# Optimization experiments

Hardware: AMD Instinct MI355X
Metric: run time of the kernel (lower is better)

Reference implementation:

```python
import jax, jax.numpy as jnp
import numpy as np

N_STEPS = 128
N_UNITS = 2048
BATCH = 256
DT = 1e-3
TAU_M = 10.0 * DT            # NeuroTorch LIFLayer default tau_m
ALPHA = float(np.exp(-DT / TAU_M))  # membrane decay factor
THRESHOLD = 1.0
GAMMA = 100.0                # surrogate-gradient sharpness


@jax.custom_vjp
def heaviside_spike(v):
    # forward: hard threshold; backward: sigmoid surrogate (see fwdbwd module)
    return (v > THRESHOLD).astype(v.dtype)

def _hs_fwd(v):
    return heaviside_spike(v), v

def _hs_bwd(v, g):
    sig = jax.nn.sigmoid(GAMMA * (v - THRESHOLD))
    return (g * GAMMA * sig * (1.0 - sig),)

heaviside_spike.defvjp(_hs_fwd, _hs_bwd)


def setup_inputs() -> dict:
    key = jax.random.key(0)
    kx, kw = jax.random.split(key)
    x = jax.random.normal(kx, (BATCH, N_UNITS), dtype=jnp.float32)
    # LIF feedforward weights (n_units -> n_units), no recurrent connection
    W = (jax.random.normal(kw, (N_UNITS, N_UNITS), dtype=jnp.float32)
         / np.float32(np.sqrt(N_UNITS)))
    return {"x": x, "W": W}


def reference(x, W):
    # x: (B, N) analog input; first "spike" frame is the raw input (as in source).
    def step(carry, _):
        x_fwd, V, Z = carry
        I = x_fwd @ W                                   # (B, N)
        # reset term uses detached spikes in the original (stop_gradient)
        V_next = ALPHA * V * (1.0 - jax.lax.stop_gradient(Z)) + I
        Z_next = heaviside_spike(V_next)
        return (Z_next, V_next, Z_next), Z_next

    V0 = jnp.zeros_like(x)
    Z0 = jnp.zeros_like(x)
    _, spikes = jax.lax.scan(step, (x, V0, Z0), None, length=N_STEPS - 1)
    # spikes: (n_steps-1, B, N); prepend the analog frame -> stack along time
    out = jnp.concatenate([x[None], spikes], axis=0)    # (T, B, N)
    return jnp.transpose(out, (1, 0, 2))                # (B, T, N)
```

## Files before the change

### kernel.cpp

```cpp
#include <hip/hip_runtime.h>
#include <stdint.h>


#define BATCHSZ 256
#define NU      2048
#define TSTEPS  128
#define BLK     1024
#define NWAVES  (BLK / 64)

#define D_BN 128
#define D_BM 8

__global__ __launch_bounds__(128) void lif_dense_v1(
    const float* __restrict__ x,
    const float* __restrict__ W,
    float* __restrict__ ws)
{
    __shared__ float s_x[D_BM * NU];

    const int tid  = threadIdx.x;
    const int lane = tid & 63;
    const int n0   = blockIdx.x * D_BN;
    const int m0   = blockIdx.y * D_BM;

    {
        const float4* xg = (const float4*)(x + (size_t)m0 * NU);
        float4*       xs = (float4*)s_x;
        #pragma unroll
        for (int j = 0; j < 32; ++j)
            xs[j * 128 + tid] = xg[j * 128 + tid];
    }
    __syncthreads();

    const int rb = (tid >> 6) * 4;
    const float* xw = &s_x[rb * NU];

    const float* wp = W + n0 + lane * 2;

    float2 bA[16], bB[16];
    float2 acc[4];
    #pragma unroll
    for (int r = 0; r < 4; ++r) { acc[r].x = 0.0f; acc[r].y = 0.0f; }

    #pragma unroll
    for (int j = 0; j < 16; ++j)
        bA[j] = *(const float2*)(wp + (size_t)j * NU);

    for (int k0 = 0; k0 < NU; k0 += 32) {
        #pragma unroll
        for (int j = 0; j < 16; ++j)
            bB[j] = *(const float2*)(wp + (size_t)(k0 + 16 + j) * NU);

        #pragma unroll
        for (int q = 0; q < 4; ++q) {
            float4 xq[4];
            #pragma unroll
            for (int r = 0; r < 4; ++r)
                xq[r] = *(const float4*)&xw[r * NU + k0 + q * 4];
            const float* xf = (const float*)&xq[0];
            #pragma unroll
            for (int kk = 0; kk < 4; ++kk) {
                float2 wv = bA[q * 4 + kk];
                #pragma unroll
                for (int r = 0; r < 4; ++r) {
                    float xv = xf[r * 4 + kk];
                    acc[r].x = __builtin_fmaf(xv, wv.x, acc[r].x);
                    acc[r].y = __builtin_fmaf(xv, wv.y, acc[r].y);
                }
            }
        }

        if (k0 + 32 < NU) {
            #pragma unroll
            for (int j = 0; j < 16; ++j)
                bA[j] = *(const float2*)(wp + (size_t)(k0 + 32 + j) * NU);
        }

        #pragma unroll
        for (int q = 0; q < 4; ++q) {
            float4 xq[4];
            #pragma unroll
            for (int r = 0; r < 4; ++r)
                xq[r] = *(const float4*)&xw[r * NU + k0 + 16 + q * 4];
            const float* xf = (const float*)&xq[0];
            #pragma unroll
            for (int kk = 0; kk < 4; ++kk) {
                float2 wv = bB[q * 4 + kk];
                #pragma unroll
                for (int r = 0; r < 4; ++r) {
                    float xv = xf[r * 4 + kk];
                    acc[r].x = __builtin_fmaf(xv, wv.x, acc[r].x);
                    acc[r].y = __builtin_fmaf(xv, wv.y, acc[r].y);
                }
            }
        }
    }

    #pragma unroll
    for (int r = 0; r < 4; ++r)
        *(float2*)&ws[(size_t)(m0 + rb + r) * NU + n0 + lane * 2] = acc[r];
}

__global__ __launch_bounds__(BLK) void lif_recurrence(
    const float* __restrict__ x,
    const float* __restrict__ W,
    const float* __restrict__ V1,
    float* __restrict__ out)
{
    const int b    = blockIdx.x;
    const int tid  = threadIdx.x;
    const int lane = tid & 63;
    const int wid  = tid >> 6;

    __shared__ int           s_idx[NU];
    __shared__ unsigned char s_flag[NU];
    __shared__ int           s_wsum[NWAVES];
    __shared__ int           s_cnt;

    const int n0 = tid;
    const int n1 = tid + BLK;

    float* outb = out + (size_t)b * TSTEPS * NU;

    float V0, V1r;
    int   z0, z1;
    {
        float x0 = x[(size_t)b * NU + n0];
        float x1 = x[(size_t)b * NU + n1];
        outb[n0] = x0;
        outb[n1] = x1;
        V0  = V1[(size_t)b * NU + n0];
        V1r = V1[(size_t)b * NU + n1];
        z0 = V0  > 1.0f;
        z1 = V1r > 1.0f;
        float* f1 = outb + NU;
        f1[n0] = z0 ? 1.0f : 0.0f;
        f1[n1] = z1 ? 1.0f : 0.0f;
        s_flag[n0] = (unsigned char)z0;
        s_flag[n1] = (unsigned char)z1;
    }
    __syncthreads();

    for (int t = 2; t < TSTEPS; ++t) {
        int f0 = s_flag[2 * tid];
        int f1 = s_flag[2 * tid + 1];
        int c  = f0 + f1;
        int v  = c;
        #pragma unroll
        for (int d = 1; d < 64; d <<= 1) {
            int o = __shfl_up(v, d);
            if (lane >= d) v += o;
        }
        if (lane == 63) s_wsum[wid] = v;
        __syncthreads();
        int base = 0;
        #pragma unroll
        for (int w = 0; w < NWAVES; ++w) base += (w < wid) ? s_wsum[w] : 0;
        int off = base + v - c;
        if (f0) s_idx[off++] = (2 * tid) * NU;
        if (f1) s_idx[off]   = (2 * tid + 1) * NU;
        if (tid == BLK - 1) s_cnt = base + v;
        __syncthreads();

        int cnt = s_cnt;
        if (cnt == 0) {
            size_t  elems  = (size_t)(TSTEPS - t) * NU;
            float4* p      = (float4*)(outb + (size_t)t * NU);
            int     chunks = (int)(elems / 4);
            float4  zz; zz.x = zz.y = zz.z = zz.w = 0.0f;
            for (int i = tid; i < chunks; i += BLK) p[i] = zz;
            return;
        }

        float I0 = 0.0f, I1 = 0.0f;
        const float* Wc = W + tid;
        int i = 0;
        for (; i + 4 <= cnt; i += 4) {
            const float* r0 = Wc + s_idx[i];
            const float* r1 = Wc + s_idx[i + 1];
            const float* r2 = Wc + s_idx[i + 2];
            const float* r3 = Wc + s_idx[i + 3];
            float a0 = r0[0], b0 = r0[BLK];
            float a1 = r1[0], b1 = r1[BLK];
            float a2 = r2[0], b2 = r2[BLK];
            float a3 = r3[0], b3 = r3[BLK];
            I0 += a0; I0 += a1; I0 += a2; I0 += a3;
            I1 += b0; I1 += b1; I1 += b2; I1 += b3;
        }
        for (; i < cnt; ++i) {
            const float* r = Wc + s_idx[i];
            I0 += r[0];
            I1 += r[BLK];
        }

        float d0 = 0.90483741803595952f * V0;
        float d1 = 0.90483741803595952f * V1r;
        asm volatile("" : "+v"(d0), "+v"(d1));
        float nv0 = (z0 ? 0.0f : d0) + I0;
        float nv1 = (z1 ? 0.0f : d1) + I1;
        V0 = nv0; V1r = nv1;
        z0 = nv0 > 1.0f;
        z1 = nv1 > 1.0f;

        float* po = outb + (size_t)t * NU;
        po[n0] = z0 ? 1.0f : 0.0f;
        po[n1] = z1 ? 1.0f : 0.0f;
        s_flag[n0] = (unsigned char)z0;
        s_flag[n1] = (unsigned char)z1;
        __syncthreads();
    }
}

__global__ __launch_bounds__(BLK) void lif_fused(
    const float* __restrict__ x,
    const float* __restrict__ W,
    float* __restrict__ out)
{
    const int b    = blockIdx.x;
    const int tid  = threadIdx.x;
    const int lane = tid & 63;
    const int wid  = tid >> 6;

    __shared__ float         s_x[NU];
    __shared__ int           s_idx[NU];
    __shared__ unsigned char s_flag[NU];
    __shared__ int           s_wsum[NWAVES];
    __shared__ int           s_cnt;

    const int n0 = tid;
    const int n1 = tid + BLK;
    float* outb = out + (size_t)b * TSTEPS * NU;

    {
        float x0 = x[(size_t)b * NU + n0];
        float x1 = x[(size_t)b * NU + n1];
        s_x[n0] = x0; s_x[n1] = x1;
        outb[n0] = x0; outb[n1] = x1;
    }
    __syncthreads();

    float I0 = 0.0f, I1 = 0.0f;
    {
        const float* Wc = W + tid;
        #pragma unroll 8
        for (int k = 0; k < NU; ++k) {
            float xk = s_x[k];
            const float* wr = Wc + (size_t)k * NU;
            I0 = __builtin_fmaf(xk, wr[0],   I0);
            I1 = __builtin_fmaf(xk, wr[BLK], I1);
        }
    }

    float V0 = 0.0f, V1 = 0.0f;
    int   z0 = 0,    z1 = 0;

    for (int t = 1; t < TSTEPS; ++t) {
        if (t >= 2) {
            int f0 = s_flag[2 * tid];
            int f1 = s_flag[2 * tid + 1];
            int c  = f0 + f1;
            int v  = c;
            #pragma unroll
            for (int d = 1; d < 64; d <<= 1) {
                int o = __shfl_up(v, d);
                if (lane >= d) v += o;
            }
            if (lane == 63) s_wsum[wid] = v;
            __syncthreads();
            int base = 0;
            #pragma unroll
            for (int w = 0; w < NWAVES; ++w) base += (w < wid) ? s_wsum[w] : 0;
            int off = base + v - c;
            if (f0) s_idx[off++] = 2 * tid;
            if (f1) s_idx[off]   = 2 * tid + 1;
            if (tid == BLK - 1) s_cnt = base + v;
            __syncthreads();

            int cnt = s_cnt;
            if (cnt == 0) {
                size_t  elems  = (size_t)(TSTEPS - t) * NU;
                float4* p      = (float4*)(outb + (size_t)t * NU);
                int     chunks = (int)(elems / 4);
                float4  zz; zz.x = zz.y = zz.z = zz.w = 0.0f;
                for (int i = tid; i < chunks; i += BLK) p[i] = zz;
                return;
            }

            I0 = 0.0f; I1 = 0.0f;
            const float* Wc = W + tid;
            int i = 0;
            for (; i + 2 <= cnt; i += 2) {
                const float* r0 = Wc + (size_t)s_idx[i]     * NU;
                const float* r1 = Wc + (size_t)s_idx[i + 1] * NU;
                float a0 = r0[0], b0 = r0[BLK];
                float a1 = r1[0], b1 = r1[BLK];
                I0 += a0; I0 += a1;
                I1 += b0; I1 += b1;
            }
            for (; i < cnt; ++i) {
                const float* r = Wc + (size_t)s_idx[i] * NU;
                I0 += r[0];
                I1 += r[BLK];
            }
        }

        float d0 = 0.90483741803595952f * V0;
        float d1 = 0.90483741803595952f * V1;
        asm volatile("" : "+v"(d0), "+v"(d1));
        float nv0 = (z0 ? 0.0f : d0) + I0;
        float nv1 = (z1 ? 0.0f : d1) + I1;
        V0 = nv0; V1 = nv1;
        z0 = nv0 > 1.0f;
        z1 = nv1 > 1.0f;

        float* po = outb + (size_t)t * NU;
        po[n0] = z0 ? 1.0f : 0.0f;
        po[n1] = z1 ? 1.0f : 0.0f;
        s_flag[n0] = (unsigned char)z0;
        s_flag[n1] = (unsigned char)z1;
        __syncthreads();
    }
}

extern "C" void kernel_launch(void* const* d_in, const int* in_sizes, int n_in,
                              void* d_out, int out_size, void* d_ws, size_t ws_size,
                              hipStream_t stream) {
    const float* x = (const float*)d_in[0];
    const float* W = (const float*)d_in[1];
    if (n_in >= 2 && in_sizes[0] == NU * NU && in_sizes[1] == BATCHSZ * NU) {
        const float* t = x; x = W; W = t;
    }
    float* out = (float*)d_out;

    const size_t need = (size_t)BATCHSZ * NU * sizeof(float);
    if (ws_size >= need) {
        float* V1 = (float*)d_ws;
        hipLaunchKernelGGL(lif_dense_v1,
                           dim3(NU / D_BN, BATCHSZ / D_BM), dim3(128), 0, stream,
                           x, W, V1);
        hipLaunchKernelGGL(lif_recurrence,
                           dim3(BATCHSZ), dim3(BLK), 0, stream,
                           x, W, V1, out);
    } else {
        hipLaunchKernelGGL(lif_fused, dim3(BATCHSZ), dim3(BLK), 0, stream,
                           x, W, out);
    }
}
```

Measured before the change: 193.5 us.

## Remap dense GEMM blocks per XCD and double-buffer shared-memory x fragments

The first-step dense GEMM now uses a 1D grid of 512 blocks, remapped so that each of the 8 XCDs gets two adjacent N tiles across all M tiles. Blocks on the same XCD then share W columns in its L2. The x operand fragments are also prefetched from LDS into register double buffers, next to the existing W double buffering, so LDS latency overlaps with FMAs. This raises register pressure (32 float4 plus 32 float2 buffers), which may lower occupancy. The dense kernel is only a small part of the total next to the 127-step recurrence kernel.

Result: faster. 168.4 us (-13.0%).

```diff
diff --git a/kernel.cpp b/kernel.cpp
--- a/kernel.cpp
+++ b/kernel.cpp
@@ -20,8 +20,14 @@
 
     const int tid  = threadIdx.x;
     const int lane = tid & 63;
-    const int n0   = blockIdx.x * D_BN;
-    const int m0   = blockIdx.y * D_BM;
+
+    const int bid    = blockIdx.x;
+    const int xcd    = bid & 7;
+    const int w      = bid >> 3;
+    const int n_tile = xcd * 2 + (w >> 5);
+    const int m_tile = w & 31;
+    const int n0     = n_tile * D_BN;
+    const int m0     = m_tile * D_BM;
 
     {
         const float4* xg = (const float4*)(x + (size_t)m0 * NU);
@@ -34,66 +40,69 @@
 
     const int rb = (tid >> 6) * 4;
     const float* xw = &s_x[rb * NU];
-
     const float* wp = W + n0 + lane * 2;
 
-    float2 bA[16], bB[16];
+    float2 wA[16], wB[16];
+    float4 xA[16], xB[16];
     float2 acc[4];
     #pragma unroll
     for (int r = 0; r < 4; ++r) { acc[r].x = 0.0f; acc[r].y = 0.0f; }
 
     #pragma unroll
     for (int j = 0; j < 16; ++j)
-        bA[j] = *(const float2*)(wp + (size_t)j * NU);
+        wA[j] = *(const float2*)(wp + (size_t)j * NU);
+    #pragma unroll
+    for (int q = 0; q < 4; ++q)
+        #pragma unroll
+        for (int r = 0; r < 4; ++r)
+            xA[q * 4 + r] = *(const float4*)&xw[r * NU + q * 4];
 
     for (int k0 = 0; k0 < NU; k0 += 32) {
         #pragma unroll
         for (int j = 0; j < 16; ++j)
-            bB[j] = *(const float2*)(wp + (size_t)(k0 + 16 + j) * NU);
-
-        #pragma unroll
-        for (int q = 0; q < 4; ++q) {
-            float4 xq[4];
+            wB[j] = *(const float2*)(wp + (size_t)(k0 + 16 + j) * NU);
+        #pragma unroll
+        for (int q = 0; q < 4; ++q)
             #pragma unroll
             for (int r = 0; r < 4; ++r)
-                xq[r] = *(const float4*)&xw[r * NU + k0 + q * 4];
-            const float* xf = (const float*)&xq[0];
+                xB[q * 4 + r] = *(const float4*)&xw[r * NU + k0 + 16 + q * 4];
+
+        #pragma unroll
+        for (int q = 0; q < 4; ++q)
             #pragma unroll
             for (int kk = 0; kk < 4; ++kk) {
-                float2 wv = bA[q * 4 + kk];
+                float2 wv = wA[q * 4 + kk];
                 #pragma unroll
                 for (int r = 0; r < 4; ++r) {
-                    float xv = xf[r * 4 + kk];
+                    float xv = ((const float*)&xA[q * 4 + r])[kk];
                     acc[r].x = __builtin_fmaf(xv, wv.x, acc[r].x);
                     acc[r].y = __builtin_fmaf(xv, wv.y, acc[r].y);
                 }
             }
-        }
 
         if (k0 + 32 < NU) {
             #pragma unroll
             for (int j = 0; j < 16; ++j)
-                bA[j] = *(const float2*)(wp + (size_t)(k0 + 32 + j) * NU);
-        }
-
-        #pragma unroll
-        for (int q = 0; q < 4; ++q) {
-            float4 xq[4];
-            #pragma unroll
-            for (int r = 0; r < 4; ++r)
-                xq[r] = *(const float4*)&xw[r * NU + k0 + 16 + q * 4];
-            const float* xf = (const float*)&xq[0];
+                wA[j] = *(const float2*)(wp + (size_t)(k0 + 32 + j) * NU);
+            #pragma unroll
+            for (int q = 0; q < 4; ++q)
+                #pragma unroll
+                for (int r = 0; r < 4; ++r)
+                    xA[q * 4 + r] = *(const float4*)&xw[r * NU + k0 + 32 + q * 4];
+        }
+
+        #pragma unroll
+        for (int q = 0; q < 4; ++q)
             #pragma unroll
             for (int kk = 0; kk < 4; ++kk) {
-                float2 wv = bB[q * 4 + kk];
+                float2 wv = wB[q * 4 + kk];
                 #pragma unroll
                 for (int r = 0; r < 4; ++r) {
-                    float xv = xf[r * 4 + kk];
+                    float xv = ((const float*)&xB[q * 4 + r])[kk];
                     acc[r].x = __builtin_fmaf(xv, wv.x, acc[r].x);
                     acc[r].y = __builtin_fmaf(xv, wv.y, acc[r].y);
                 }
             }
-        }
     }
 
     #pragma unroll
@@ -336,7 +345,7 @@
     if (ws_size >= need) {
         float* V1 = (float*)d_ws;
         hipLaunchKernelGGL(lif_dense_v1,
-                           dim3(NU / D_BN, BATCHSZ / D_BM), dim3(128), 0, stream,
+                           dim3(512), dim3(128), 0, stream,
                            x, W, V1);
         hipLaunchKernelGGL(lif_recurrence,
                            dim3(BATCHSZ), dim3(BLK), 0, stream,
```
